# Optimization experiments

Hardware: AMD Instinct MI355X
Metric: run time of the kernel (lower is better)

Reference implementation:

```python
import jax, jax.numpy as jnp
import numpy as np

N = 100000   # nodes
E = 1600000  # edges
H = 128      # hidden_channels
G = 2        # group
D = H // G   # per-group channels
L = 2        # num_layers
T = 112      # num_tasks
MSG_EPS = 1e-7


def _ln(x, g, b):
    mu = jnp.mean(x, axis=-1, keepdims=True)
    var = jnp.var(x, axis=-1, keepdims=True)
    return (x - mu) * jax.lax.rsqrt(var + 1e-5) * g + b


def setup_inputs() -> dict:
    key = jax.random.key(0)
    ks = jax.random.split(key, 12)
    s8, s16, sH, sD = 1/np.sqrt(8), 1/np.sqrt(16), 1/np.sqrt(H), 1/np.sqrt(D)
    inp = {}
    inp["x"] = jax.random.uniform(ks[0], (N, 8), jnp.float32)
    inp["node_index"] = jax.random.randint(ks[1], (N,), 0, N)
    inp["edge_index"] = jax.random.randint(ks[2], (2, E), 0, N)
    inp["edge_attr"] = jax.random.uniform(ks[3], (E, 8), jnp.float32)
    inp["node_features"] = jax.random.normal(ks[4], (N, 8), jnp.float32)
    inp["W_oh"] = jax.random.normal(ks[5], (8, 8)) * s8
    inp["b_oh"] = jnp.zeros((8,))
    inp["W_ne"] = jax.random.normal(ks[6], (16, H)) * s16
    inp["b_ne"] = jnp.zeros((H,))
    inp["W_ee"] = jax.random.normal(ks[7], (8, H)) * s8
    inp["b_ee"] = jnp.zeros((H,))
    inp["ln_g"] = jnp.ones((L, G, D))
    inp["ln_b"] = jnp.zeros((L, G, D))
    inp["We"] = jax.random.normal(ks[8], (L, G, H, D)) * sH   # GENConv edge encoder per Fm
    inp["be"] = jnp.zeros((L, G, D))
    inp["Wm"] = jax.random.normal(ks[9], (L, G, D, D)) * sD   # GENConv 1-layer MLP
    inp["bm"] = jnp.zeros((L, G, D))
    inp["last_g"] = jnp.ones((H,))
    inp["last_b"] = jnp.zeros((H,))
    inp["Wp"] = jax.random.normal(ks[10], (H, T)) * sH
    inp["bp"] = jnp.zeros((T,))
    return inp


def _gen_block(y_in, src, dst, ee, g, b, We_, be_, Wm_, bm_):
    # GENBlock (res+ pre-activation): norm -> relu -> GENConv(softmax aggr, t=1)
    h = jax.nn.relu(_ln(y_in, g, b))                       # [N,D]
    msg = jax.nn.relu(h[src] + ee @ We_ + be_) + MSG_EPS   # [E,D]
    mx = jax.lax.stop_gradient(jax.ops.segment_max(msg, dst, num_segments=N))
    mx = jnp.where(jnp.isfinite(mx), mx, 0.0)
    ex = jnp.exp(msg - mx[dst])
    den = jax.ops.segment_sum(ex, dst, num_segments=N)
    w = ex / (den[dst] + 1e-16)                            # scatter_softmax weights
    agg = jax.ops.segment_sum(msg * w, dst, num_segments=N)  # [N,D]
    return (h + agg) @ Wm_ + bm_


def reference(x, node_index, edge_index, edge_attr, node_features, W_oh, b_oh, W_ne, b_ne, W_ee, b_ee, ln_g, ln_b, We, be, Wm, bm, last_g, last_b, Wp, bp):
    nf1 = node_features[node_index]                        # [N,8]
    nf2 = x @ W_oh + b_oh                                  # one-hot encoder [N,8]
    h = jnp.concatenate([nf1, nf2], axis=1) @ W_ne + b_ne  # [N,H]
    ee = edge_attr @ W_ee + b_ee                           # [E,H]; cat of G copies chunks back to identical [E,H]
    src, dst = edge_index[0], edge_index[1]
    for l in range(L):
        # GroupAdditiveCoupling (group=2): y_i = x_i + F_i(y_{i-1})
        x1, x2 = jnp.split(h, G, axis=-1)
        y1 = x1 + _gen_block(x2, src, dst, ee, ln_g[l, 0], ln_b[l, 0], We[l, 0], be[l, 0], Wm[l, 0], bm[l, 0])
        y2 = x2 + _gen_block(y1, src, dst, ee, ln_g[l, 1], ln_b[l, 1], We[l, 1], be[l, 1], Wm[l, 1], bm[l, 1])
        h = jnp.concatenate([y1, y2], axis=-1)
    h = jax.nn.relu(_ln(h, last_g, last_b))
    return h @ Wp + bp
```

## Files before the change

### kernel.cpp

```cpp
#include <hip/hip_runtime.h>

constexpr int N_NODES = 100000;
constexpr int N_EDGES = 1600000;
constexpr int T_OUT = 112;

constexpr int SCAN_CHUNK = 1024;
constexpr int SCAN_BLOCKS = (N_NODES + SCAN_CHUNK - 1) / SCAN_CHUNK;

typedef _Float16 h2v __attribute__((ext_vector_type(2)));
typedef _Float16 half4 __attribute__((ext_vector_type(4)));
typedef _Float16 half8 __attribute__((ext_vector_type(8)));
typedef float f32x4 __attribute__((ext_vector_type(4)));
typedef int i4v __attribute__((ext_vector_type(4)));
typedef float f4v __attribute__((ext_vector_type(4)));

__device__ __forceinline__ float dot2h(h2v a, h2v b, float c) {
#if __has_builtin(__builtin_amdgcn_fdot2)
    return __builtin_amdgcn_fdot2(a, b, c, false);
#else
    return fmaf((float)a.x, (float)b.x, fmaf((float)a.y, (float)b.y, c));
#endif
}
__device__ __forceinline__ int pk2(float a, float b) {
    auto v = __builtin_amdgcn_cvt_pkrtz(a, b);
    return __builtin_bit_cast(int, v);
}
__device__ __forceinline__ h2v b2h(int x) { return __builtin_bit_cast(h2v, x); }
__device__ __forceinline__ unsigned short f2h(float f) {
    return __builtin_bit_cast(unsigned short, (_Float16)f);
}
__device__ __forceinline__ float h2f(unsigned short u) {
    return (float)__builtin_bit_cast(_Float16, u);
}

__global__ void wcomb_kernel(const float* __restrict__ W_ee,
                             const float* __restrict__ b_ee,
                             const float* __restrict__ We,
                             const float* __restrict__ be,
                             int* __restrict__ Wc_h2,
                             float* __restrict__ bcomb) {
    int lg = blockIdx.x;
    int d = threadIdx.x;
    const float* We_ = We + (size_t)lg * 128 * 64;
    float acc[9];
#pragma unroll
    for (int k = 0; k < 9; ++k) acc[k] = 0.f;
    for (int c = 0; c < 128; ++c) {
        float wv = We_[c * 64 + d];
#pragma unroll
        for (int k = 0; k < 8; ++k) acc[k] += W_ee[k * 128 + c] * wv;
        acc[8] += b_ee[c] * wv;
    }
#pragma unroll
    for (int j = 0; j < 4; ++j)
        Wc_h2[lg * 256 + j * 64 + d] = pk2(acc[2 * j], acc[2 * j + 1]);
    bcomb[lg * 64 + d] = acc[8] + be[lg * 64 + d];
}

__global__ void wp_pack_kernel(const float* __restrict__ Wp, int* __restrict__ wpfrag) {
    int tm = blockIdx.x;
    int tile = tm >> 2, m = tm & 3;
    int lane = threadIdx.x;
    int g = lane >> 4, r = lane & 15;
    int t = tile * 16 + r;
    int o[4];
#pragma unroll
    for (int p = 0; p < 4; ++p) {
        int j0 = 2 * p, j1 = 2 * p + 1;
        int k0 = m * 32 + (j0 >> 2) * 16 + g * 4 + (j0 & 3);
        int k1 = m * 32 + (j1 >> 2) * 16 + g * 4 + (j1 & 3);
        o[p] = pk2(Wp[k0 * 112 + t], Wp[k1 * 112 + t]);
    }
    int4 o4; o4.x = o[0]; o4.y = o[1]; o4.z = o[2]; o4.w = o[3];
    *(int4*)(wpfrag + ((size_t)tm * 64 + lane) * 4) = o4;
}

__global__ void wm_pack_kernel(const float* __restrict__ Wm, int* __restrict__ wmfrag) {
    int b = blockIdx.x;
    int lg = b >> 3, tm = b & 7;
    int tile = tm >> 1, m = tm & 1;
    int lane = threadIdx.x;
    int g = lane >> 4, r = lane & 15;
    const float* W = Wm + (size_t)lg * 4096;
    int col = tile * 16 + r;
    int o[4];
#pragma unroll
    for (int p = 0; p < 4; ++p) {
        int j0 = 2 * p, j1 = 2 * p + 1;
        int k0 = m * 32 + (j0 >> 2) * 16 + g * 4 + (j0 & 3);
        int k1 = m * 32 + (j1 >> 2) * 16 + g * 4 + (j1 & 3);
        o[p] = pk2(W[k0 * 64 + col], W[k1 * 64 + col]);
    }
    int4 o4; o4.x = o[0]; o4.y = o[1]; o4.z = o[2]; o4.w = o[3];
    *(int4*)(wmfrag + ((size_t)b * 64 + lane) * 4) = o4;
}

__global__ __launch_bounds__(256) void encoder_kernel(
    const float* __restrict__ x, const int* __restrict__ node_index,
    const float* __restrict__ node_features,
    const float* __restrict__ W_oh, const float* __restrict__ b_oh,
    const float* __restrict__ W_ne, const float* __restrict__ b_ne,
    float* __restrict__ A, float* __restrict__ B) {
    int tid = threadIdx.x;
    int w = tid >> 6, d = tid & 63;
    int n = blockIdx.x * 4 + w;

    float xf[8];
    const float* xr = x + (size_t)n * 8;
#pragma unroll
    for (int j = 0; j < 8; ++j) xf[j] = xr[j];

    float nf[16];
    int ni = node_index[n];
    const float* nfr = node_features + (size_t)ni * 8;
#pragma unroll
    for (int k = 0; k < 8; ++k) nf[k] = nfr[k];
#pragma unroll
    for (int k = 0; k < 8; ++k) {
        float acc = b_oh[k];
#pragma unroll
        for (int j = 0; j < 8; ++j) acc += xf[j] * W_oh[j * 8 + k];
        nf[8 + k] = acc;
    }
    float hA = b_ne[d], hB = b_ne[64 + d];
#pragma unroll
    for (int k = 0; k < 16; ++k) {
        hA += nf[k] * W_ne[k * 128 + d];
        hB += nf[k] * W_ne[k * 128 + 64 + d];
    }
    A[(size_t)n * 64 + d] = hA;
    B[(size_t)n * 64 + d] = hB;
}

__global__ void hist_kernel(const int* __restrict__ edge_index,
                            int* __restrict__ deg, int* __restrict__ rank) {
    int e = blockIdx.x * 256 + threadIdx.x;
    if (e < N_EDGES) rank[e] = atomicAdd(&deg[edge_index[N_EDGES + e]], 1);
}

__global__ __launch_bounds__(256) void block_sum_kernel(const int* __restrict__ deg,
                                                        int* __restrict__ blocksum) {
    __shared__ int s_w[4];
    int t = threadIdx.x;
    int base = blockIdx.x * SCAN_CHUNK + t * 4;
    int s = 0;
    if (base + 3 < N_NODES) {
        int4 v = *(const int4*)(deg + base);
        s = v.x + v.y + v.z + v.w;
    } else {
        for (int j = 0; j < 4; ++j)
            if (base + j < N_NODES) s += deg[base + j];
    }
#pragma unroll
    for (int o = 32; o >= 1; o >>= 1) s += __shfl_xor(s, o, 64);
    if ((t & 63) == 0) s_w[t >> 6] = s;
    __syncthreads();
    if (t == 0) blocksum[blockIdx.x] = s_w[0] + s_w[1] + s_w[2] + s_w[3];
}

__global__ __launch_bounds__(64) void scan_sums_kernel(const int* __restrict__ blocksum,
                                                       int* __restrict__ blockoff,
                                                       int* __restrict__ rowptr) {
    int t = threadIdx.x;
    int i0 = 2 * t, i1 = 2 * t + 1;
    int v0 = (i0 < SCAN_BLOCKS) ? blocksum[i0] : 0;
    int v1 = (i1 < SCAN_BLOCKS) ? blocksum[i1] : 0;
    int s = v0 + v1;
    int incl = s;
#pragma unroll
    for (int o = 1; o < 64; o <<= 1) {
        int u = __shfl_up(incl, o, 64);
        if (t >= o) incl += u;
    }
    int excl = incl - s;
    if (i0 < SCAN_BLOCKS) blockoff[i0] = excl;
    if (i1 < SCAN_BLOCKS) blockoff[i1] = excl + v0;
    if (t == 63) rowptr[N_NODES] = incl;
}

__global__ __launch_bounds__(256) void emit_kernel(const int* __restrict__ deg,
                                                   const int* __restrict__ blockoff,
                                                   int* __restrict__ rowptr) {
    __shared__ int s_w[4];
    int t = threadIdx.x;
    int w = t >> 6, lane = t & 63;
    int base = blockIdx.x * SCAN_CHUNK + t * 4;

    int d0 = 0, d1 = 0, d2 = 0, d3 = 0;
    if (base + 3 < N_NODES) {
        int4 v = *(const int4*)(deg + base);
        d0 = v.x; d1 = v.y; d2 = v.z; d3 = v.w;
    } else {
        if (base + 0 < N_NODES) d0 = deg[base + 0];
        if (base + 1 < N_NODES) d1 = deg[base + 1];
        if (base + 2 < N_NODES) d2 = deg[base + 2];
        if (base + 3 < N_NODES) d3 = deg[base + 3];
    }
    int s = d0 + d1 + d2 + d3;
    int incl = s;
#pragma unroll
    for (int o = 1; o < 64; o <<= 1) {
        int u = __shfl_up(incl, o, 64);
        if (lane >= o) incl += u;
    }
    if (lane == 63) s_w[w] = incl;
    __syncthreads();
    int woff = 0;
    for (int j = 0; j < 4; ++j) woff += (j < w) ? s_w[j] : 0;

    int p = blockoff[blockIdx.x] + woff + incl - s;
    int4 r;
    r.x = p;
    r.y = p + d0;
    r.z = p + d0 + d1;
    r.w = p + d0 + d1 + d2;
    if (base + 3 < N_NODES) {
        *(int4*)(rowptr + base) = r;
    } else {
        if (base + 0 < N_NODES) rowptr[base + 0] = r.x;
        if (base + 1 < N_NODES) rowptr[base + 1] = r.y;
        if (base + 2 < N_NODES) rowptr[base + 2] = r.z;
        if (base + 3 < N_NODES) rowptr[base + 3] = r.w;
    }
}

__global__ void scatter_kernel(const int* __restrict__ edge_index,
                               const float* __restrict__ edge_attr,
                               const int* __restrict__ rowptr,
                               const int* __restrict__ rank,
                               int* __restrict__ src_perm,
                               int* __restrict__ ea_h) {
    int e = blockIdx.x * 256 + threadIdx.x;
    if (e >= N_EDGES) return;
    int dn = edge_index[N_EDGES + e];
    int idx = rowptr[dn] + rank[e];
    f4v a = __builtin_nontemporal_load((const f4v*)(edge_attr + (size_t)e * 8));
    f4v b = __builtin_nontemporal_load((const f4v*)(edge_attr + (size_t)e * 8 + 4));
    i4v o;
    o.x = pk2(a.x, a.y);
    o.y = pk2(a.z, a.w);
    o.z = pk2(b.x, b.y);
    o.w = pk2(b.z, b.w);
    __builtin_nontemporal_store(o, (i4v*)(ea_h + (size_t)idx * 4));
    __builtin_nontemporal_store(edge_index[e], src_perm + idx);
}

__global__ __launch_bounds__(256) void ln_relu_kernel(const float* __restrict__ Y,
                                                      const float* __restrict__ g,
                                                      const float* __restrict__ b,
                                                      unsigned short* __restrict__ hl16) {
    int tid = threadIdx.x;
    int w = tid >> 6, d = tid & 63;
    int n = blockIdx.x * 4 + w;
    float y = Y[(size_t)n * 64 + d];
    float s = y, sq = y * y;
#pragma unroll
    for (int offd = 32; offd >= 1; offd >>= 1) {
        s += __shfl_xor(s, offd, 64);
        sq += __shfl_xor(sq, offd, 64);
    }
    float mean = s * (1.f / 64.f);
    float var = sq * (1.f / 64.f) - mean * mean;
    float rs = rsqrtf(var + 1e-5f);
    float h = (y - mean) * rs * g[d] + b[d];
    hl16[(size_t)n * 64 + d] = f2h(fmaxf(h, 0.f));
}

__global__ __launch_bounds__(256) void agg_kernel(
    const unsigned short* __restrict__ hl_in, unsigned short* __restrict__ v16,
    const int* __restrict__ rowptr, const int* __restrict__ src_perm,
    const int* __restrict__ ea_h,
    const int* __restrict__ Wc_h2, const float* __restrict__ bcomb) {
    int tid = threadIdx.x;
    int w = tid >> 6, d = tid & 63;
    int n = __builtin_amdgcn_readfirstlane(blockIdx.x * 4 + w);

    h2v wcA = b2h(Wc_h2[0 * 64 + d]);
    h2v wcB = b2h(Wc_h2[1 * 64 + d]);
    h2v wcC = b2h(Wc_h2[2 * 64 + d]);
    h2v wcD = b2h(Wc_h2[3 * 64 + d]);
    float bc = bcomb[d];

    float num = 0.f, den = 0.f;
    int start = rowptr[n], end = rowptr[n + 1];
    const int4* ea4 = (const int4*)ea_h;

#define RFL(X) __builtin_amdgcn_readfirstlane(X)
#define EDGE(U, E)                                                    \
    {                                                                 \
        float eW = bc;                                                \
        eW = dot2h(b2h(E.x), wcA, eW);                                \
        eW = dot2h(b2h(E.y), wcB, eW);                                \
        eW = dot2h(b2h(E.z), wcC, eW);                                \
        eW = dot2h(b2h(E.w), wcD, eW);                                \
        float m = fmaxf(h2f(U) + eW, 0.f) + 1e-7f;                    \
        float ex = __expf(m);                                         \
        den += ex;                                                    \
        num += ex * m;                                                \
    }

    int i = start;
    for (; i + 8 <= end; i += 8) {
        int s0 = RFL(src_perm[i + 0]), s1 = RFL(src_perm[i + 1]);
        int s2 = RFL(src_perm[i + 2]), s3 = RFL(src_perm[i + 3]);
        int s4 = RFL(src_perm[i + 4]), s5 = RFL(src_perm[i + 5]);
        int s6 = RFL(src_perm[i + 6]), s7 = RFL(src_perm[i + 7]);
        unsigned short u0 = hl_in[(size_t)s0 * 64 + d];
        unsigned short u1 = hl_in[(size_t)s1 * 64 + d];
        unsigned short u2 = hl_in[(size_t)s2 * 64 + d];
        unsigned short u3 = hl_in[(size_t)s3 * 64 + d];
        unsigned short u4 = hl_in[(size_t)s4 * 64 + d];
        unsigned short u5 = hl_in[(size_t)s5 * 64 + d];
        unsigned short u6 = hl_in[(size_t)s6 * 64 + d];
        unsigned short u7 = hl_in[(size_t)s7 * 64 + d];
        int4 e0 = ea4[i + 0], e1 = ea4[i + 1], e2 = ea4[i + 2], e3 = ea4[i + 3];
        EDGE(u0, e0) EDGE(u1, e1) EDGE(u2, e2) EDGE(u3, e3)
        int4 e4 = ea4[i + 4], e5 = ea4[i + 5], e6 = ea4[i + 6], e7 = ea4[i + 7];
        EDGE(u4, e4) EDGE(u5, e5) EDGE(u6, e6) EDGE(u7, e7)
    }
    for (; i + 4 <= end; i += 4) {
        int s0 = RFL(src_perm[i + 0]), s1 = RFL(src_perm[i + 1]);
        int s2 = RFL(src_perm[i + 2]), s3 = RFL(src_perm[i + 3]);
        unsigned short u0 = hl_in[(size_t)s0 * 64 + d];
        unsigned short u1 = hl_in[(size_t)s1 * 64 + d];
        unsigned short u2 = hl_in[(size_t)s2 * 64 + d];
        unsigned short u3 = hl_in[(size_t)s3 * 64 + d];
        int4 e0 = ea4[i + 0], e1 = ea4[i + 1], e2 = ea4[i + 2], e3 = ea4[i + 3];
        EDGE(u0, e0) EDGE(u1, e1) EDGE(u2, e2) EDGE(u3, e3)
    }
    for (; i < end; ++i) {
        int s0 = RFL(src_perm[i]);
        unsigned short u0 = hl_in[(size_t)s0 * 64 + d];
        int4 e0 = ea4[i];
        EDGE(u0, e0)
    }
#undef EDGE
#undef RFL

    float agg = num / (den + 1e-16f);
    float v = h2f(hl_in[(size_t)n * 64 + d]) + agg;
    v16[(size_t)n * 64 + d] = f2h(v);
}

template <bool PRODUCE_HL>
__global__ __launch_bounds__(256) void epi_kernel(
    const unsigned short* __restrict__ v16, float* __restrict__ Y,
    const int* __restrict__ wmfrag, const float* __restrict__ bm,
    const float* __restrict__ gnext, const float* __restrict__ bnext,
    unsigned short* __restrict__ hl_out) {
    int tid = threadIdx.x;
    int w = tid >> 6, lane = tid & 63;
    int g = lane >> 4, r = lane & 15;
    int nodebase = blockIdx.x * 64 + w * 16;
    if (nodebase >= N_NODES) return;

    const unsigned short* vp = v16 + (size_t)(nodebase + r) * 64;
    half8 af[2];
#pragma unroll
    for (int m = 0; m < 2; ++m) {
        int k0 = m * 32 + g * 4;
        half4 lo = *(const half4*)(vp + k0);
        half4 hi = *(const half4*)(vp + k0 + 16);
        af[m][0] = lo[0]; af[m][1] = lo[1]; af[m][2] = lo[2]; af[m][3] = lo[3];
        af[m][4] = hi[0]; af[m][5] = hi[1]; af[m][6] = hi[2]; af[m][7] = hi[3];
    }

    const int4* wf4 = (const int4*)wmfrag;
    f32x4 acc[4];
#pragma unroll
    for (int tile = 0; tile < 4; ++tile) {
        float bmv = bm[tile * 16 + r];
        acc[tile] = {bmv, bmv, bmv, bmv};
#pragma unroll
        for (int m = 0; m < 2; ++m) {
            int4 bw = wf4[(tile * 2 + m) * 64 + lane];
            half8 bf = __builtin_bit_cast(half8, bw);
            acc[tile] = __builtin_amdgcn_mfma_f32_16x16x32_f16(af[m], bf, acc[tile], 0, 0, 0);
        }
    }

    float yn[4][4];
#pragma unroll
    for (int tile = 0; tile < 4; ++tile) {
#pragma unroll
        for (int q = 0; q < 4; ++q) {
            size_t idx = (size_t)(nodebase + g * 4 + q) * 64 + tile * 16 + r;
            float y = Y[idx] + acc[tile][q];
            yn[tile][q] = y;
            Y[idx] = y;
        }
    }

    if constexpr (PRODUCE_HL) {
        float gnv[4], bnv[4];
#pragma unroll
        for (int tile = 0; tile < 4; ++tile) {
            gnv[tile] = gnext[tile * 16 + r];
            bnv[tile] = bnext[tile * 16 + r];
        }
#pragma unroll
        for (int q = 0; q < 4; ++q) {
            float s = yn[0][q] + yn[1][q] + yn[2][q] + yn[3][q];
            float sq = yn[0][q] * yn[0][q] + yn[1][q] * yn[1][q]
                     + yn[2][q] * yn[2][q] + yn[3][q] * yn[3][q];
            s += __shfl_xor(s, 1, 64);  sq += __shfl_xor(sq, 1, 64);
            s += __shfl_xor(s, 2, 64);  sq += __shfl_xor(sq, 2, 64);
            s += __shfl_xor(s, 4, 64);  sq += __shfl_xor(sq, 4, 64);
            s += __shfl_xor(s, 8, 64);  sq += __shfl_xor(sq, 8, 64);
            float mean = s * (1.f / 64.f);
            float var = sq * (1.f / 64.f) - mean * mean;
            float rs = rsqrtf(var + 1e-5f);
#pragma unroll
            for (int tile = 0; tile < 4; ++tile) {
                float h = (yn[tile][q] - mean) * rs * gnv[tile] + bnv[tile];
                hl_out[(size_t)(nodebase + g * 4 + q) * 64 + tile * 16 + r] =
                    f2h(fmaxf(h, 0.f));
            }
        }
    }
}

__global__ __launch_bounds__(256) void final_kernel(
    const float* __restrict__ A, const float* __restrict__ B,
    const float* __restrict__ lg, const float* __restrict__ lb,
    const int* __restrict__ wpfrag, const float* __restrict__ bp,
    float* __restrict__ out) {
    int tid = threadIdx.x;
    int w = tid >> 6, lane = tid & 63;
    int g = lane >> 4, r = lane & 15;
    int nodebase = blockIdx.x * 64 + w * 16;
    if (nodebase >= N_NODES) return;
    int n = nodebase + r;

    float4 v[8];
    const float4* A4 = (const float4*)(A + (size_t)n * 64);
    const float4* B4 = (const float4*)(B + (size_t)n * 64);
#pragma unroll
    for (int kb = 0; kb < 4; ++kb) v[kb] = A4[kb * 4 + g];
#pragma unroll
    for (int kb = 0; kb < 4; ++kb) v[4 + kb] = B4[kb * 4 + g];

    float s = 0.f, sq = 0.f;
#pragma unroll
    for (int kb = 0; kb < 8; ++kb) {
        s += v[kb].x + v[kb].y + v[kb].z + v[kb].w;
        sq += v[kb].x * v[kb].x + v[kb].y * v[kb].y
            + v[kb].z * v[kb].z + v[kb].w * v[kb].w;
    }
    s += __shfl_xor(s, 16, 64);  sq += __shfl_xor(sq, 16, 64);
    s += __shfl_xor(s, 32, 64);  sq += __shfl_xor(sq, 32, 64);
    float mean = s * (1.f / 128.f);
    float var = sq * (1.f / 128.f) - mean * mean;
    float rs = rsqrtf(var + 1e-5f);

    const float4* lg4 = (const float4*)lg;
    const float4* lb4 = (const float4*)lb;
    half8 afr[4];
#pragma unroll
    for (int kb = 0; kb < 8; ++kb) {
        float4 gv = lg4[kb * 4 + g];
        float4 bv = lb4[kb * 4 + g];
        int m = kb >> 1, e0 = (kb & 1) * 4;
        afr[m][e0 + 0] = (_Float16)fmaxf((v[kb].x - mean) * rs * gv.x + bv.x, 0.f);
        afr[m][e0 + 1] = (_Float16)fmaxf((v[kb].y - mean) * rs * gv.y + bv.y, 0.f);
        afr[m][e0 + 2] = (_Float16)fmaxf((v[kb].z - mean) * rs * gv.z + bv.z, 0.f);
        afr[m][e0 + 3] = (_Float16)fmaxf((v[kb].w - mean) * rs * gv.w + bv.w, 0.f);
    }

    const int4* wf4 = (const int4*)wpfrag;
#pragma unroll
    for (int tile = 0; tile < 7; ++tile) {
        float bias = bp[tile * 16 + r];
        f32x4 acc = {bias, bias, bias, bias};
#pragma unroll
        for (int m = 0; m < 4; ++m) {
            int4 bw = wf4[(tile * 4 + m) * 64 + lane];
            half8 bf = __builtin_bit_cast(half8, bw);
            acc = __builtin_amdgcn_mfma_f32_16x16x32_f16(afr[m], bf, acc, 0, 0, 0);
        }
#pragma unroll
        for (int q = 0; q < 4; ++q) {
            out[(size_t)(nodebase + g * 4 + q) * T_OUT + tile * 16 + r] = acc[q];
        }
    }
}

extern "C" void kernel_launch(void* const* d_in, const int* in_sizes, int n_in,
                              void* d_out, int out_size, void* d_ws, size_t ws_size,
                              hipStream_t stream) {
    const float* x            = (const float*)d_in[0];
    const int* node_index     = (const int*)d_in[1];
    const int* edge_index     = (const int*)d_in[2];
    const float* edge_attr    = (const float*)d_in[3];
    const float* node_features= (const float*)d_in[4];
    const float* W_oh         = (const float*)d_in[5];
    const float* b_oh         = (const float*)d_in[6];
    const float* W_ne         = (const float*)d_in[7];
    const float* b_ne         = (const float*)d_in[8];
    const float* W_ee         = (const float*)d_in[9];
    const float* b_ee         = (const float*)d_in[10];
    const float* ln_g         = (const float*)d_in[11];
    const float* ln_b         = (const float*)d_in[12];
    const float* We           = (const float*)d_in[13];
    const float* be           = (const float*)d_in[14];
    const float* Wm           = (const float*)d_in[15];
    const float* bm           = (const float*)d_in[16];
    const float* last_g       = (const float*)d_in[17];
    const float* last_b       = (const float*)d_in[18];
    const float* Wp           = (const float*)d_in[19];
    const float* bp           = (const float*)d_in[20];
    float* out = (float*)d_out;

    char* ws = (char*)d_ws;
    size_t off = 0;
    auto alloc = [&](size_t bytes) -> void* {
        void* p = ws + off;
        off = (off + bytes + 255) & ~(size_t)255;
        return p;
    };
    float* A          = (float*)alloc((size_t)N_NODES * 64 * 4);
    float* B          = (float*)alloc((size_t)N_NODES * 64 * 4);
    unsigned short* hl = (unsigned short*)alloc((size_t)N_NODES * 64 * 2);
    unsigned short* v16 = (unsigned short*)alloc((size_t)N_NODES * 64 * 2);
    int* deg          = (int*)alloc((size_t)N_NODES * 4);
    int* rowptr       = (int*)alloc((size_t)(N_NODES + 1) * 4);
    int* rank         = (int*)alloc((size_t)N_EDGES * 4);
    int* src_perm     = (int*)alloc((size_t)N_EDGES * 4);
    int* ea_h         = (int*)alloc((size_t)N_EDGES * 4 * 4);
    int* Wc_h2        = (int*)alloc(4 * 256 * 4);
    float* bcomb      = (float*)alloc(4 * 64 * 4);
    int* blocksum     = (int*)alloc((size_t)SCAN_BLOCKS * 4);
    int* blockoff     = (int*)alloc((size_t)SCAN_BLOCKS * 4);
    int* wpfrag       = (int*)alloc((size_t)28 * 64 * 16);
    int* wmfrag       = (int*)alloc((size_t)32 * 64 * 16);
    (void)ws_size; (void)in_sizes; (void)n_in; (void)out_size;

    const int NB_NODE = N_NODES / 4;
    const int NB_EDGE = (N_EDGES + 255) / 256;
    const int NB_EPI  = (N_NODES + 63) / 64;

    (void)hipMemsetAsync(deg, 0, (size_t)N_NODES * 4, stream);
    wcomb_kernel<<<4, 64, 0, stream>>>(W_ee, b_ee, We, be, Wc_h2, bcomb);
    wp_pack_kernel<<<28, 64, 0, stream>>>(Wp, wpfrag);
    wm_pack_kernel<<<32, 64, 0, stream>>>(Wm, wmfrag);
    encoder_kernel<<<NB_NODE, 256, 0, stream>>>(x, node_index, node_features,
                                                W_oh, b_oh, W_ne, b_ne, A, B);
    hist_kernel<<<NB_EDGE, 256, 0, stream>>>(edge_index, deg, rank);
    block_sum_kernel<<<SCAN_BLOCKS, 256, 0, stream>>>(deg, blocksum);
    scan_sums_kernel<<<1, 64, 0, stream>>>(blocksum, blockoff, rowptr);
    emit_kernel<<<SCAN_BLOCKS, 256, 0, stream>>>(deg, blockoff, rowptr);
    scatter_kernel<<<NB_EDGE, 256, 0, stream>>>(edge_index, edge_attr, rowptr,
                                                rank, src_perm, ea_h);

    ln_relu_kernel<<<NB_NODE, 256, 0, stream>>>(B, ln_g, ln_b, hl);

    agg_kernel<<<NB_NODE, 256, 0, stream>>>(hl, v16, rowptr, src_perm, ea_h,
                                            Wc_h2 + 0 * 256, bcomb + 0 * 64);
    epi_kernel<true><<<NB_EPI, 256, 0, stream>>>(
        v16, A, wmfrag + 0 * 8 * 256, bm + 0 * 64,
        ln_g + 1 * 64, ln_b + 1 * 64, hl);
    agg_kernel<<<NB_NODE, 256, 0, stream>>>(hl, v16, rowptr, src_perm, ea_h,
                                            Wc_h2 + 1 * 256, bcomb + 1 * 64);
    epi_kernel<true><<<NB_EPI, 256, 0, stream>>>(
        v16, B, wmfrag + 1 * 8 * 256, bm + 1 * 64,
        ln_g + 2 * 64, ln_b + 2 * 64, hl);
    agg_kernel<<<NB_NODE, 256, 0, stream>>>(hl, v16, rowptr, src_perm, ea_h,
                                            Wc_h2 + 2 * 256, bcomb + 2 * 64);
    epi_kernel<true><<<NB_EPI, 256, 0, stream>>>(
        v16, A, wmfrag + 2 * 8 * 256, bm + 2 * 64,
        ln_g + 3 * 64, ln_b + 3 * 64, hl);
    agg_kernel<<<NB_NODE, 256, 0, stream>>>(hl, v16, rowptr, src_perm, ea_h,
                                            Wc_h2 + 3 * 256, bcomb + 3 * 64);
    epi_kernel<false><<<NB_EPI, 256, 0, stream>>>(
        v16, B, wmfrag + 3 * 8 * 256, bm + 3 * 64,
        nullptr, nullptr, nullptr);

    final_kernel<<<NB_EPI, 256, 0, stream>>>(A, B, last_g, last_b, wpfrag, bp, out);
}
```

Before: 611.6 us.

## Process two channels per lane so each wavefront aggregates two nodes

The softmax aggregation kernel now maps a half-wavefront of 32 lanes to each destination node, with every lane handling two adjacent channels via 32-bit packed half loads. A 256-thread block covers 8 nodes instead of 4, and the grid is halved to match. This cuts the number of gather instructions and spreads the per-edge scalar index and edge-attribute loads over more work per wave. The trade-off is that source indices are no longer readfirstlane-uniform, because the two halves of a wave walk different edge lists. It also adds divergence when neighbouring nodes have different degrees, and drops the 8-way unroll.

```diff
diff --git a/kernel.cpp b/kernel.cpp
--- a/kernel.cpp
+++ b/kernel.cpp
@@ -272,74 +272,69 @@
     const int* __restrict__ ea_h,
     const int* __restrict__ Wc_h2, const float* __restrict__ bcomb) {
     int tid = threadIdx.x;
-    int w = tid >> 6, d = tid & 63;
-    int n = __builtin_amdgcn_readfirstlane(blockIdx.x * 4 + w);
-
-    h2v wcA = b2h(Wc_h2[0 * 64 + d]);
-    h2v wcB = b2h(Wc_h2[1 * 64 + d]);
-    h2v wcC = b2h(Wc_h2[2 * 64 + d]);
-    h2v wcD = b2h(Wc_h2[3 * 64 + d]);
-    float bc = bcomb[d];
-
-    float num = 0.f, den = 0.f;
+    int w = tid >> 6, lane = tid & 63;
+    int half = lane >> 5;
+    int c = (lane & 31) * 2;
+    int n = blockIdx.x * 8 + w * 2 + half;
+
+    h2v wc0[4], wc1[4];
+#pragma unroll
+    for (int j = 0; j < 4; ++j) {
+        wc0[j] = b2h(Wc_h2[j * 64 + c]);
+        wc1[j] = b2h(Wc_h2[j * 64 + c + 1]);
+    }
+    float bc0 = bcomb[c], bc1 = bcomb[c + 1];
+
+    float num0 = 0.f, den0 = 0.f, num1 = 0.f, den1 = 0.f;
     int start = rowptr[n], end = rowptr[n + 1];
     const int4* ea4 = (const int4*)ea_h;
 
-#define RFL(X) __builtin_amdgcn_readfirstlane(X)
-#define EDGE(U, E)                                                    \
-    {                                                                 \
-        float eW = bc;                                                \
-        eW = dot2h(b2h(E.x), wcA, eW);                                \
-        eW = dot2h(b2h(E.y), wcB, eW);                                \
-        eW = dot2h(b2h(E.z), wcC, eW);                                \
-        eW = dot2h(b2h(E.w), wcD, eW);                                \
-        float m = fmaxf(h2f(U) + eW, 0.f) + 1e-7f;                    \
-        float ex = __expf(m);                                         \
-        den += ex;                                                    \
-        num += ex * m;                                                \
+#define EDGE(U, E)                                                        \
+    {                                                                     \
+        h2v hv = b2h((int)(U));                                           \
+        float eW0 = bc0, eW1 = bc1;                                       \
+        eW0 = dot2h(b2h(E.x), wc0[0], eW0);                               \
+        eW1 = dot2h(b2h(E.x), wc1[0], eW1);                               \
+        eW0 = dot2h(b2h(E.y), wc0[1], eW0);                               \
+        eW1 = dot2h(b2h(E.y), wc1[1], eW1);                               \
+        eW0 = dot2h(b2h(E.z), wc0[2], eW0);                               \
+        eW1 = dot2h(b2h(E.z), wc1[2], eW1);                               \
+        eW0 = dot2h(b2h(E.w), wc0[3], eW0);                               \
+        eW1 = dot2h(b2h(E.w), wc1[3], eW1);                               \
+        float m0 = fmaxf((float)hv.x + eW0, 0.f) + 1e-7f;                 \
+        float m1 = fmaxf((float)hv.y + eW1, 0.f) + 1e-7f;                 \
+        float x0 = __expf(m0), x1 = __expf(m1);                           \
+        den0 += x0; num0 += x0 * m0;                                      \
+        den1 += x1; num1 += x1 * m1;                                      \
     }
 
     int i = start;
-    for (; i + 8 <= end; i += 8) {
-        int s0 = RFL(src_perm[i + 0]), s1 = RFL(src_perm[i + 1]);
-        int s2 = RFL(src_perm[i + 2]), s3 = RFL(src_perm[i + 3]);
-        int s4 = RFL(src_perm[i + 4]), s5 = RFL(src_perm[i + 5]);
-        int s6 = RFL(src_perm[i + 6]), s7 = RFL(src_perm[i + 7]);
-        unsigned short u0 = hl_in[(size_t)s0 * 64 + d];
-        unsigned short u1 = hl_in[(size_t)s1 * 64 + d];
-        unsigned short u2 = hl_in[(size_t)s2 * 64 + d];
-        unsigned short u3 = hl_in[(size_t)s3 * 64 + d];
-        unsigned short u4 = hl_in[(size_t)s4 * 64 + d];
-        unsigned short u5 = hl_in[(size_t)s5 * 64 + d];
-        unsigned short u6 = hl_in[(size_t)s6 * 64 + d];
-        unsigned short u7 = hl_in[(size_t)s7 * 64 + d];
+    for (; i + 4 <= end; i += 4) {
+        int s0 = src_perm[i + 0];
+        int s1 = src_perm[i + 1];
+        int s2 = src_perm[i + 2];
+        int s3 = src_perm[i + 3];
+        unsigned int u0 = *(const unsigned int*)(hl_in + (size_t)s0 * 64 + c);
+        unsigned int u1 = *(const unsigned int*)(hl_in + (size_t)s1 * 64 + c);
+        unsigned int u2 = *(const unsigned int*)(hl_in + (size_t)s2 * 64 + c);
+        unsigned int u3 = *(const unsigned int*)(hl_in + (size_t)s3 * 64 + c);
         int4 e0 = ea4[i + 0], e1 = ea4[i + 1], e2 = ea4[i + 2], e3 = ea4[i + 3];
         EDGE(u0, e0) EDGE(u1, e1) EDGE(u2, e2) EDGE(u3, e3)
-        int4 e4 = ea4[i + 4], e5 = ea4[i + 5], e6 = ea4[i + 6], e7 = ea4[i + 7];
-        EDGE(u4, e4) EDGE(u5, e5) EDGE(u6, e6) EDGE(u7, e7)
-    }
-    for (; i + 4 <= end; i += 4) {
-        int s0 = RFL(src_perm[i + 0]), s1 = RFL(src_perm[i + 1]);
-        int s2 = RFL(src_perm[i + 2]), s3 = RFL(src_perm[i + 3]);
-        unsigned short u0 = hl_in[(size_t)s0 * 64 + d];
-        unsigned short u1 = hl_in[(size_t)s1 * 64 + d];
-        unsigned short u2 = hl_in[(size_t)s2 * 64 + d];
-        unsigned short u3 = hl_in[(size_t)s3 * 64 + d];
-        int4 e0 = ea4[i + 0], e1 = ea4[i + 1], e2 = ea4[i + 2], e3 = ea4[i + 3];
-        EDGE(u0, e0) EDGE(u1, e1) EDGE(u2, e2) EDGE(u3, e3)
     }
     for (; i < end; ++i) {
-        int s0 = RFL(src_perm[i]);
-        unsigned short u0 = hl_in[(size_t)s0 * 64 + d];
+        int s0 = src_perm[i];
+        unsigned int u0 = *(const unsigned int*)(hl_in + (size_t)s0 * 64 + c);
         int4 e0 = ea4[i];
         EDGE(u0, e0)
     }
 #undef EDGE
-#undef RFL
-
-    float agg = num / (den + 1e-16f);
-    float v = h2f(hl_in[(size_t)n * 64 + d]) + agg;
-    v16[(size_t)n * 64 + d] = f2h(v);
+
+    float agg0 = num0 / (den0 + 1e-16f);
+    float agg1 = num1 / (den1 + 1e-16f);
+    unsigned int uself = *(const unsigned int*)(hl_in + (size_t)n * 64 + c);
+    h2v sv = b2h((int)uself);
+    int vout = pk2((float)sv.x + agg0, (float)sv.y + agg1);
+    *(int*)(v16 + (size_t)n * 64 + c) = vout;
 }
 
 template <bool PRODUCE_HL>
@@ -537,6 +532,7 @@
 
     const int NB_NODE = N_NODES / 4;
     const int NB_EDGE = (N_EDGES + 255) / 256;
+    const int NB_AGG  = N_NODES / 8;
     const int NB_EPI  = (N_NODES + 63) / 64;
 
     (void)hipMemsetAsync(deg, 0, (size_t)N_NODES * 4, stream);
@@ -554,23 +550,23 @@
 
     ln_relu_kernel<<<NB_NODE, 256, 0, stream>>>(B, ln_g, ln_b, hl);
 
-    agg_kernel<<<NB_NODE, 256, 0, stream>>>(hl, v16, rowptr, src_perm, ea_h,
-                                            Wc_h2 + 0 * 256, bcomb + 0 * 64);
+    agg_kernel<<<NB_AGG, 256, 0, stream>>>(hl, v16, rowptr, src_perm, ea_h,
+                                           Wc_h2 + 0 * 256, bcomb + 0 * 64);
     epi_kernel<true><<<NB_EPI, 256, 0, stream>>>(
         v16, A, wmfrag + 0 * 8 * 256, bm + 0 * 64,
         ln_g + 1 * 64, ln_b + 1 * 64, hl);
-    agg_kernel<<<NB_NODE, 256, 0, stream>>>(hl, v16, rowptr, src_perm, ea_h,
-                                            Wc_h2 + 1 * 256, bcomb + 1 * 64);
+    agg_kernel<<<NB_AGG, 256, 0, stream>>>(hl, v16, rowptr, src_perm, ea_h,
+                                           Wc_h2 + 1 * 256, bcomb + 1 * 64);
     epi_kernel<true><<<NB_EPI, 256, 0, stream>>>(
         v16, B, wmfrag + 1 * 8 * 256, bm + 1 * 64,
         ln_g + 2 * 64, ln_b + 2 * 64, hl);
-    agg_kernel<<<NB_NODE, 256, 0, stream>>>(hl, v16, rowptr, src_perm, ea_h,
-                                            Wc_h2 + 2 * 256, bcomb + 2 * 64);
+    agg_kernel<<<NB_AGG, 256, 0, stream>>>(hl, v16, rowptr, src_perm, ea_h,
+                                           Wc_h2 + 2 * 256, bcomb + 2 * 64);
     epi_kernel<true><<<NB_EPI, 256, 0, stream>>>(
         v16, A, wmfrag + 2 * 8 * 256, bm + 2 * 64,
         ln_g + 3 * 64, ln_b + 3 * 64, hl);
-    agg_kernel<<<NB_NODE, 256, 0, stream>>>(hl, v16, rowptr, src_perm, ea_h,
-                                            Wc_h2 + 3 * 256, bcomb + 3 * 64);
+    agg_kernel<<<NB_AGG, 256, 0, stream>>>(hl, v16, rowptr, src_perm, ea_h,
+                                           Wc_h2 + 3 * 256, bcomb + 3 * 64);
     epi_kernel<false><<<NB_EPI, 256, 0, stream>>>(
         v16, B, wmfrag + 3 * 8 * 256, bm + 3 * 64,
         nullptr, nullptr, nullptr);
```

Result: no change. 608.0 us (-0.6%).
